# Optimization experiments

Measured on AMD Instinct MI355X. Metric: run time of the kernel, lower is better.

Reference implementation:

```python
import jax, jax.numpy as jnp
import numpy as np

N, D, H = 3072, 1152, 16
HD = D // H  # 72


def setup_inputs() -> dict:
    key = jax.random.key(0)
    ks = jax.random.split(key, 12)
    w = lambda k, shp: jax.random.normal(k, shp, dtype=jnp.float32) * 0.02
    return {
        "hidden_states": jax.random.normal(ks[0], (N, D), dtype=jnp.float32),
        "rotary_pos_emb": jax.random.normal(ks[1], (N, HD // 2), dtype=jnp.float32),
        "cu_seqlens": jnp.arange(5, dtype=jnp.int32) * (N // 4),
        "wq": w(ks[2], (D, D)), "bq": jnp.zeros((D,), jnp.float32),
        "wk": w(ks[3], (D, D)), "bk": jnp.zeros((D,), jnp.float32),
        "wv": w(ks[4], (D, D)), "bv": jnp.zeros((D,), jnp.float32),
        "wo": w(ks[5], (D, D)), "bo": jnp.zeros((D,), jnp.float32),
    }


def _rotate_half(x):
    x1, x2 = jnp.split(x, 2, axis=-1)
    return jnp.concatenate((-x2, x1), axis=-1)


def _apply_rope(t, freqs):
    # t: [N, H, HD], freqs: [N, HD//2]
    cos = jnp.concatenate([jnp.cos(freqs), jnp.cos(freqs)], axis=-1)[:, None, :]  # [N,1,HD]
    sin = jnp.concatenate([jnp.sin(freqs), jnp.sin(freqs)], axis=-1)[:, None, :]
    return (t.astype(jnp.float32) * cos + _rotate_half(t.astype(jnp.float32)) * sin).astype(t.dtype)


def reference(hidden_states, rotary_pos_emb, cu_seqlens, wq, bq, wk, bk, wv, bv, wo, bo):
    n = hidden_states.shape[0]
    q = (hidden_states @ wq.T + bq).reshape(n, H, HD)
    k = (hidden_states @ wk.T + bk).reshape(n, H, HD)
    v = (hidden_states @ wv.T + bv).reshape(n, H, HD)
    q = _apply_rope(q, rotary_pos_emb)
    k = _apply_rope(k, rotary_pos_emb)
    # block-diagonal mask: same segment id (from cu_seqlens) -> attend
    seg = jnp.searchsorted(cu_seqlens, jnp.arange(n), side="right")
    same = seg[:, None] == seg[None, :]  # [N, N]
    neg = jnp.finfo(q.dtype).min
    scores = jnp.einsum("qhd,khd->hqk", q, k) / jnp.sqrt(jnp.float32(HD)).astype(q.dtype)
    scores = scores + jnp.where(same, jnp.zeros((), q.dtype), neg)[None, :, :]
    attn = jax.nn.softmax(scores.astype(jnp.float32), axis=-1).astype(q.dtype)
    out = jnp.einsum("hqk,khd->qhd", attn, v).reshape(n, D)
    return out @ wo.T + bo
```

## Files before the change

kernel.cpp:

```cpp
#include <hip/hip_runtime.h>
#include <hip/hip_bf16.h>


typedef __attribute__((ext_vector_type(8))) __bf16 bf16x8;
typedef __attribute__((ext_vector_type(4))) float f32x4;
typedef __attribute__((ext_vector_type(8))) unsigned short u16x8;
typedef __attribute__((ext_vector_type(4))) unsigned short u16x4;

#define N_TOK 3072
#define DMODEL 1152
#define NH 16
#define HDIM 72
#define SEGLEN 768

__device__ __forceinline__ unsigned short bf16rn(float f) {
  union { float f; unsigned int u; } v; v.f = f;
  return (unsigned short)((v.u + 0x7fffu + ((v.u >> 16) & 1u)) >> 16);
}
__device__ __forceinline__ float bf2f(unsigned short u) {
  union { unsigned int i; float f; } v; v.i = ((unsigned int)u) << 16;
  return v.f;
}

#define GLOAD16(gsrc, ldst)                                                  \
  __builtin_amdgcn_global_load_lds(                                         \
      (const __attribute__((address_space(1))) unsigned int*)(gsrc),        \
      (__attribute__((address_space(3))) unsigned int*)(ldst), 16, 0, 0)

template <int N> __device__ __forceinline__ void waitcnt_vm() {
  if constexpr (N == 0) asm volatile("s_waitcnt vmcnt(0)" ::: "memory");
  else if constexpr (N == 2) asm volatile("s_waitcnt vmcnt(2)" ::: "memory");
  else if constexpr (N == 3) asm volatile("s_waitcnt vmcnt(3)" ::: "memory");
  else if constexpr (N == 4) asm volatile("s_waitcnt vmcnt(4)" ::: "memory");
}

__global__ __launch_bounds__(256) void prep_kernel(
    const float* __restrict__ hs,
    const float* __restrict__ wq, const float* __restrict__ wk,
    const float* __restrict__ wv, const float* __restrict__ wo,
    const float* __restrict__ bq, const float* __restrict__ bk,
    const float* __restrict__ bv,
    unsigned short* __restrict__ Xbf, unsigned short* __restrict__ Wqkv,
    unsigned short* __restrict__ Wo, float* __restrict__ biasqkv) {
  const int idx = blockIdx.x * 256 + threadIdx.x;
  const int stride = gridDim.x * 256;
  const int NX4 = (N_TOK * DMODEL) / 4;
  const int NW4 = (DMODEL * DMODEL) / 4;
  for (int i = idx; i < NX4; i += stride) {
    f32x4 v = ((const f32x4*)hs)[i];
    u16x4 o;
    for (int j = 0; j < 4; ++j) o[j] = bf16rn(v[j]);
    ((u16x4*)Xbf)[i] = o;
  }
  for (int i = idx; i < NW4; i += stride) {
    f32x4 a = ((const f32x4*)wq)[i];
    f32x4 b = ((const f32x4*)wk)[i];
    f32x4 c = ((const f32x4*)wv)[i];
    f32x4 d = ((const f32x4*)wo)[i];
    u16x4 oa, ob, oc, od;
    for (int j = 0; j < 4; ++j) {
      oa[j] = bf16rn(a[j]); ob[j] = bf16rn(b[j]);
      oc[j] = bf16rn(c[j]); od[j] = bf16rn(d[j]);
    }
    ((u16x4*)Wqkv)[i] = oa;
    ((u16x4*)(Wqkv + DMODEL * DMODEL))[i] = ob;
    ((u16x4*)(Wqkv + 2 * DMODEL * DMODEL))[i] = oc;
    ((u16x4*)Wo)[i] = od;
  }
  for (int i = idx; i < DMODEL; i += stride) {
    biasqkv[i] = bq[i];
    biasqkv[DMODEL + i] = bk[i];
    biasqkv[2 * DMODEL + i] = bv[i];
  }
}

template <int BM, int BN, int FM, int FN, bool OBF>
__global__ __launch_bounds__(256) void gemm_lds_kernel(
    const unsigned short* __restrict__ A, const unsigned short* __restrict__ B,
    const float* __restrict__ bias, void* __restrict__ Cout,
    int Nout, int K, int nbx) {
  __shared__ unsigned short As[3][BM * 32];
  __shared__ unsigned short Bs[3][BN * 32];
  const int t = threadIdx.x;
  const int lane = t & 63, wave = t >> 6;
  const int wr = wave >> 1, wc = wave & 1;
  const int g = lane >> 4, li = lane & 15;
  constexpr int LPS = BM / 64 + BN / 64;

  const int per = gridDim.x >> 3;
  const int gb = (blockIdx.x & 7) * per + (blockIdx.x >> 3);
  const int by = gb / nbx, bx = gb - by * nbx;
  const int bm = by * BM, bn = bx * BN;

  constexpr int LA = BM / 64;
  constexpr int LB = BN / 64;

  auto stage = [&](int buf, int kt) {
#pragma unroll
    for (int i = 0; i < LA; ++i) {
      const int s = i * 256 + t;
      const int row = s >> 2, cs = s & 3;
      const int gg = cs ^ ((row >> 1) & 3);
      GLOAD16(A + (long)(bm + row) * K + kt + gg * 8,
              &As[buf][(i * 256 + (t & ~63)) * 8]);
    }
#pragma unroll
    for (int i = 0; i < LB; ++i) {
      const int s = i * 256 + t;
      const int row = s >> 2, cs = s & 3;
      const int gg = cs ^ ((row >> 1) & 3);
      GLOAD16(B + (long)(bn + row) * K + kt + gg * 8,
              &Bs[buf][(i * 256 + (t & ~63)) * 8]);
    }
  };

  f32x4 acc[FM][FN];
#pragma unroll
  for (int i = 0; i < FM; ++i)
#pragma unroll
    for (int j = 0; j < FN; ++j) acc[i][j] = (f32x4)0.f;

  stage(0, 0);
  stage(1, 32);
  int cur = 0;
  const int nk = K / 32;
  for (int kt = 0; kt < nk; ++kt) {
    if (kt < nk - 1) waitcnt_vm<LPS>();
    else waitcnt_vm<0>();
    __builtin_amdgcn_s_barrier();
    if (kt + 2 < nk) {
      int nb = cur + 2; if (nb >= 3) nb -= 3;
      stage(nb, (kt + 2) * 32);
    }
    bf16x8 af[FM], bf[FN];
#pragma unroll
    for (int i = 0; i < FM; ++i) {
      const int r = wr * (BM / 2) + i * 16 + li;
      af[i] = *(const bf16x8*)&As[cur][r * 32 + ((g ^ ((r >> 1) & 3)) * 8)];
    }
#pragma unroll
    for (int j = 0; j < FN; ++j) {
      const int r = wc * (BN / 2) + j * 16 + li;
      bf[j] = *(const bf16x8*)&Bs[cur][r * 32 + ((g ^ ((r >> 1) & 3)) * 8)];
    }
    __builtin_amdgcn_s_setprio(1);
#pragma unroll
    for (int i = 0; i < FM; ++i)
#pragma unroll
      for (int j = 0; j < FN; ++j)
        acc[i][j] = __builtin_amdgcn_mfma_f32_16x16x32_bf16(af[i], bf[j],
                                                            acc[i][j], 0, 0, 0);
    __builtin_amdgcn_s_setprio(0);
    cur = (cur == 2) ? 0 : cur + 1;
  }

#pragma unroll
  for (int i = 0; i < FM; ++i) {
    const int row = bm + wr * (BM / 2) + i * 16 + g * 4;
#pragma unroll
    for (int j = 0; j < FN; ++j) {
      const int col = bn + wc * (BN / 2) + j * 16 + li;
      const float bb = bias[col];
#pragma unroll
      for (int r = 0; r < 4; ++r) {
        const float v = acc[i][j][r] + bb;
        if constexpr (OBF)
          ((unsigned short*)Cout)[(long)(row + r) * Nout + col] = bf16rn(v);
        else
          ((float*)Cout)[(long)(row + r) * Nout + col] = v;
      }
    }
  }
}

__global__ __launch_bounds__(256) void rope_pack_kernel(
    const unsigned short* __restrict__ qkv, const float* __restrict__ rope,
    unsigned short* __restrict__ Qp, unsigned short* __restrict__ Kp,
    unsigned short* __restrict__ Vt) {
  const int nb = blockIdx.x;
  const int h = blockIdx.y;
  const int n0 = nb * 64;
  const int t = threadIdx.x;
  const float qscale = 0.17002501f;
  __shared__ float cs[64][36], sn[64][36];
  __shared__ float vtile[72][65];

  for (int i = t; i < 64 * 36; i += 256) {
    const int n = i / 36, d = i % 36;
    const float f = rope[(long)(n0 + n) * 36 + d];
    cs[n][d] = __cosf(f);
    sn[n][d] = __sinf(f);
  }
  __syncthreads();

  for (int i = t; i < 64 * 9; i += 256) {
    const int n = i / 9, dq = (i % 9) * 4;
    const long base = (long)(n0 + n) * 3456 + h * HDIM;
    u16x4 q1 = *(const u16x4*)&qkv[base + dq];
    u16x4 q2 = *(const u16x4*)&qkv[base + dq + 36];
    u16x4 k1 = *(const u16x4*)&qkv[base + DMODEL + dq];
    u16x4 k2 = *(const u16x4*)&qkv[base + DMODEL + dq + 36];
    u16x4 oq1, oq2, ok1, ok2;
#pragma unroll
    for (int e = 0; e < 4; ++e) {
      const float c = cs[n][dq + e], s = sn[n][dq + e];
      float f1 = bf2f(q1[e]), f2 = bf2f(q2[e]);
      oq1[e] = bf16rn((f1 * c - f2 * s) * qscale);
      oq2[e] = bf16rn((f2 * c + f1 * s) * qscale);
      f1 = bf2f(k1[e]); f2 = bf2f(k2[e]);
      ok1[e] = bf16rn(f1 * c - f2 * s);
      ok2[e] = bf16rn(f2 * c + f1 * s);
    }
    const long ob = ((long)h * N_TOK + n0 + n) * 96;
    *(u16x4*)&Qp[ob + dq] = oq1;
    *(u16x4*)&Qp[ob + dq + 36] = oq2;
    *(u16x4*)&Kp[ob + dq] = ok1;
    *(u16x4*)&Kp[ob + dq + 36] = ok2;
  }
  for (int i = t; i < 64 * 6; i += 256) {
    const int n = i / 6, dp = HDIM + (i % 6) * 4;
    const long ob = ((long)h * N_TOK + n0 + n) * 96;
    *(u16x4*)&Qp[ob + dp] = (u16x4)0;
    *(u16x4*)&Kp[ob + dp] = (u16x4)0;
  }
  for (int i = t; i < 64 * 9; i += 256) {
    const int n = i / 9, dq = (i % 9) * 8;
    u16x8 v = *(const u16x8*)&qkv[(long)(n0 + n) * 3456 + 2 * DMODEL + h * HDIM + dq];
#pragma unroll
    for (int e = 0; e < 8; ++e) vtile[dq + e][n] = bf2f(v[e]);
  }
  __syncthreads();
  for (int i = t; i < 80 * 8; i += 256) {
    const int d = i / 8, nq = (i % 8) * 8;
    u16x8 o;
#pragma unroll
    for (int e = 0; e < 8; ++e)
      o[e] = (d < HDIM) ? bf16rn(vtile[d][nq + e])
                        : (d == HDIM ? (unsigned short)0x3F80
                                     : (unsigned short)0);
    *(u16x8*)&Vt[((long)h * 80 + d) * N_TOK + n0 + nq] = o;
  }
}

__global__ __launch_bounds__(256) void attn_kernel(
    const unsigned short* __restrict__ Qp, const unsigned short* __restrict__ Kp,
    const unsigned short* __restrict__ Vt, unsigned short* __restrict__ AO) {
  const int b = blockIdx.x;
  const int hs = b & 63, qt = b >> 6;
  const int h = hs >> 2, seg = hs & 3;
  const int t = threadIdx.x;
  const int lane = t & 63, w = t >> 6;
  const int g = lane >> 4, li = lane & 15;

  __shared__ unsigned short Ks[2][32 * 96];
  __shared__ unsigned short Vs[2][80 * 32];
  __shared__ unsigned short Ps[4][16][48];

  const int q0 = seg * SEGLEN + qt * 64;
  const unsigned short* kbase = Kp + ((long)h * N_TOK + seg * SEGLEN) * 96;
  const unsigned short* vbase = Vt + (long)h * 80 * N_TOK + seg * SEGLEN;

  auto stageK = [&](int buf, int koff) {
    {
      const int row = t / 12, c = t - row * 12;
      const int gg = c ^ ((row >> 1) & 3);
      GLOAD16(kbase + (long)(koff + row) * 96 + gg * 8,
              &Ks[buf][(t & ~63) * 8]);
    }
    if (t < 128) {
      const int s = 256 + t;
      const int row = s / 12, c = s - row * 12;
      const int gg = c ^ ((row >> 1) & 3);
      GLOAD16(kbase + (long)(koff + row) * 96 + gg * 8,
              &Ks[buf][(256 + (t & ~63)) * 8]);
    }
  };
  auto stageV = [&](int buf, int koff) {
    {
      const int row = t >> 2, ch = t & 3;
      const int gg = ch ^ ((row >> 1) & 3);
      GLOAD16(vbase + (long)row * N_TOK + koff + gg * 8,
              &Vs[buf][(t & ~63) * 8]);
    }
    if (t < 64) {
      const int s = 256 + t;
      const int row = s >> 2, ch = s & 3;
      const int gg = ch ^ ((row >> 1) & 3);
      GLOAD16(vbase + (long)row * N_TOK + koff + gg * 8,
              &Vs[buf][(256 + (t & ~63)) * 8]);
    }
  };

  bf16x8 aq[3];
  {
    const unsigned short* qsrc = Qp + ((long)h * N_TOK + q0 + w * 16 + li) * 96;
#pragma unroll
    for (int c = 0; c < 3; ++c)
      aq[c] = *(const bf16x8*)(qsrc + c * 32 + g * 8);
  }

  f32x4 accO[5];
#pragma unroll
  for (int j = 0; j < 5; ++j) accO[j] = (f32x4)0.f;

  stageK(0, 0);
  stageV(0, 0);
  int cur = 0;
  for (int kv = 0; kv < 24; ++kv) {
    __syncthreads();
    if (kv + 1 < 24) {
      stageK(cur ^ 1, (kv + 1) * 32);
      stageV(cur ^ 1, (kv + 1) * 32);
    }

    f32x4 sc[2];
#pragma unroll
    for (int f = 0; f < 2; ++f) sc[f] = (f32x4)0.f;
    __builtin_amdgcn_s_setprio(1);
#pragma unroll
    for (int c = 0; c < 3; ++c)
#pragma unroll
      for (int f = 0; f < 2; ++f) {
        const int kr = f * 16 + li;
        bf16x8 bk = *(const bf16x8*)
            &Ks[cur][kr * 96 + (((c * 4 + g) ^ ((kr >> 1) & 3)) * 8)];
        sc[f] = __builtin_amdgcn_mfma_f32_16x16x32_bf16(bk, aq[c], sc[f], 0, 0, 0);
      }
    __builtin_amdgcn_s_setprio(0);

#pragma unroll
    for (int f = 0; f < 2; ++f) {
      u16x4 pk;
#pragma unroll
      for (int r = 0; r < 4; ++r) pk[r] = bf16rn(exp2f(sc[f][r]));
      *(u16x4*)&Ps[w][li][f * 16 + g * 4] = pk;
    }

    {
      bf16x8 ap = *(const bf16x8*)&Ps[w][li][g * 8];
      __builtin_amdgcn_s_setprio(1);
#pragma unroll
      for (int j = 0; j < 5; ++j) {
        const int vr = j * 16 + li;
        bf16x8 bv = *(const bf16x8*)
            &Vs[cur][vr * 32 + ((g ^ ((vr >> 1) & 3)) * 8)];
        accO[j] = __builtin_amdgcn_mfma_f32_16x16x32_bf16(ap, bv, accO[j], 0, 0, 0);
      }
      __builtin_amdgcn_s_setprio(0);
    }
    cur ^= 1;
  }

  float rinv[4];
#pragma unroll
  for (int r = 0; r < 4; ++r)
    rinv[r] = 1.f / __shfl(accO[4][r], (lane & 48) + 8);

  const int hb = h * HDIM;
#pragma unroll
  for (int j = 0; j < 5; ++j) {
    const int d = j * 16 + li;
    if (d < HDIM) {
#pragma unroll
      for (int r = 0; r < 4; ++r) {
        const int n = q0 + w * 16 + g * 4 + r;
        AO[(long)n * DMODEL + hb + d] = bf16rn(accO[j][r] * rinv[r]);
      }
    }
  }
}

extern "C" void kernel_launch(void* const* d_in, const int* in_sizes, int n_in,
                              void* d_out, int out_size, void* d_ws,
                              size_t ws_size, hipStream_t stream) {
  const float* hs = (const float*)d_in[0];
  const float* rope = (const float*)d_in[1];
  const float* wq = (const float*)d_in[3];
  const float* bq = (const float*)d_in[4];
  const float* wk = (const float*)d_in[5];
  const float* bk = (const float*)d_in[6];
  const float* wv = (const float*)d_in[7];
  const float* bv = (const float*)d_in[8];
  const float* wo = (const float*)d_in[9];
  const float* bo = (const float*)d_in[10];
  float* out = (float*)d_out;
  char* ws = (char*)d_ws;

  unsigned short* Xbf = (unsigned short*)(ws + 0);
  unsigned short* Wqkv = (unsigned short*)(ws + 7077888);
  unsigned short* Wo = (unsigned short*)(ws + 15040512);
  float* biasqkv = (float*)(ws + 17694720);
  unsigned short* qkvb = (unsigned short*)(ws + 17708544);
  unsigned short* Qp = (unsigned short*)(ws + 38942208);
  unsigned short* Kp = (unsigned short*)(ws + 48379392);
  unsigned short* Vt = (unsigned short*)(ws + 57816576);
  unsigned short* AO = (unsigned short*)(ws + 65680896);

  prep_kernel<<<dim3(1024), dim3(256), 0, stream>>>(
      hs, wq, wk, wv, wo, bq, bk, bv, Xbf, Wqkv, Wo, biasqkv);
  gemm_lds_kernel<128, 128, 4, 4, true><<<dim3(648), dim3(256), 0, stream>>>(
      Xbf, Wqkv, biasqkv, qkvb, 3 * DMODEL, DMODEL, 27);
  rope_pack_kernel<<<dim3(48, 16), dim3(256), 0, stream>>>(
      qkvb, rope, Qp, Kp, Vt);
  attn_kernel<<<dim3(768), dim3(256), 0, stream>>>(Qp, Kp, Vt, AO);
  gemm_lds_kernel<64, 128, 2, 4, false><<<dim3(432), dim3(256), 0, stream>>>(
      AO, Wo, bo, out, DMODEL, DMODEL, 9);
}
```

Baseline: 110.3 us.

## Add dedicated 256x128 QKV GEMM kernel with interleaved prefetch and XCD remap

Replaces the generic 128x128 QKV projection GEMM with a specialized 512-thread kernel that uses 256x128 tiles, K-step 64, and double-buffered LDS with XOR swizzle. Global-to-LDS prefetches for the next tile are interleaved between MFMA groups, and s_setprio raises priority around the MFMA bursts. Blocks are remapped per XCD so that each chiplet works on neighbouring tiles. The aim is higher arithmetic intensity and fewer blocks (324 instead of 648), in exchange for more LDS per block and lower occupancy.

```diff
diff --git a/kernel.cpp b/kernel.cpp
--- a/kernel.cpp
+++ b/kernel.cpp
@@ -29,6 +29,7 @@
 
 template <int N> __device__ __forceinline__ void waitcnt_vm() {
   if constexpr (N == 0) asm volatile("s_waitcnt vmcnt(0)" ::: "memory");
+  else if constexpr (N == 1) asm volatile("s_waitcnt vmcnt(1)" ::: "memory");
   else if constexpr (N == 2) asm volatile("s_waitcnt vmcnt(2)" ::: "memory");
   else if constexpr (N == 3) asm volatile("s_waitcnt vmcnt(3)" ::: "memory");
   else if constexpr (N == 4) asm volatile("s_waitcnt vmcnt(4)" ::: "memory");
@@ -74,6 +75,137 @@
   }
 }
 
+__global__ __launch_bounds__(512) void gemm_qkv_kernel(
+    const unsigned short* __restrict__ A, const unsigned short* __restrict__ B,
+    const float* __restrict__ bias, unsigned short* __restrict__ C) {
+  constexpr int K = DMODEL;
+  constexpr int NOUT = 3 * DMODEL;
+  __shared__ unsigned short As[2][256 * 64];
+  __shared__ unsigned short Bs[2][128 * 64];
+  const int t = threadIdx.x;
+  const int lane = t & 63, w = t >> 6;
+  const int wr = w >> 1, wc = w & 1;
+  const int g = lane >> 4, li = lane & 15;
+
+  const int orig = blockIdx.x;
+  const int xcd = orig & 7, pos = orig >> 3;
+  const int gb = (xcd < 4 ? xcd * 41 : 164 + (xcd - 4) * 40) + pos;
+  const int by = gb % 12, bx = gb / 12;
+  const int bm = by * 256, bn = bx * 128;
+
+  auto stageA = [&](int buf, int ko, int q) {
+    const int s = q * 512 + t;
+    const int row = s >> 3, ch = s & 7;
+    GLOAD16(A + (long)(bm + row) * K + ko + ((ch ^ (row & 7)) * 8),
+            &As[buf][(q * 512 + (t & ~63)) * 8]);
+  };
+  auto stageB = [&](int buf, int ko, int hf) {
+    const int s = hf * 512 + t;
+    const int row = s >> 3, ch = s & 7;
+    GLOAD16(B + (long)(bn + row) * K + ko + ((ch ^ (row & 7)) * 8),
+            &Bs[buf][(hf * 512 + (t & ~63)) * 8]);
+  };
+  auto rdA = [&](int buf, int i, int ks) -> bf16x8 {
+    const int r = wr * 64 + i * 16 + li;
+    return *(const bf16x8*)&As[buf][r * 64 + ((((ks << 2) + g) ^ (r & 7)) * 8)];
+  };
+  auto rdB = [&](int buf, int j, int ks) -> bf16x8 {
+    const int r = wc * 64 + j * 16 + li;
+    return *(const bf16x8*)&Bs[buf][r * 64 + ((((ks << 2) + g) ^ (r & 7)) * 8)];
+  };
+
+  f32x4 acc[4][4];
+#pragma unroll
+  for (int i = 0; i < 4; ++i)
+#pragma unroll
+    for (int j = 0; j < 4; ++j) acc[i][j] = (f32x4)0.f;
+
+  stageA(0, 0, 0); stageA(0, 0, 1); stageA(0, 0, 2); stageA(0, 0, 3);
+  stageB(0, 0, 0); stageB(0, 0, 1);
+
+  for (int kt = 0; kt < 18; ++kt) {
+    const int buf = kt & 1;
+    const bool pf = kt < 17;
+    const int ko = (kt + 1) * 64;
+    if (pf) {
+      stageA(buf ^ 1, ko, 0);
+      stageA(buf ^ 1, ko, 1);
+      waitcnt_vm<2>();
+    } else {
+      waitcnt_vm<0>();
+    }
+    __builtin_amdgcn_s_barrier();
+
+    bf16x8 b0, b1, b2, b3, a0, a1;
+    b0 = rdB(buf, 0, 0); b1 = rdB(buf, 1, 0);
+    b2 = rdB(buf, 2, 0); b3 = rdB(buf, 3, 0);
+    a0 = rdA(buf, 0, 0); a1 = rdA(buf, 1, 0);
+    if (pf) stageA(buf ^ 1, ko, 2);
+    __builtin_amdgcn_s_setprio(1);
+    acc[0][0] = __builtin_amdgcn_mfma_f32_16x16x32_bf16(a0, b0, acc[0][0], 0, 0, 0);
+    acc[0][1] = __builtin_amdgcn_mfma_f32_16x16x32_bf16(a0, b1, acc[0][1], 0, 0, 0);
+    acc[0][2] = __builtin_amdgcn_mfma_f32_16x16x32_bf16(a0, b2, acc[0][2], 0, 0, 0);
+    acc[0][3] = __builtin_amdgcn_mfma_f32_16x16x32_bf16(a0, b3, acc[0][3], 0, 0, 0);
+    acc[1][0] = __builtin_amdgcn_mfma_f32_16x16x32_bf16(a1, b0, acc[1][0], 0, 0, 0);
+    acc[1][1] = __builtin_amdgcn_mfma_f32_16x16x32_bf16(a1, b1, acc[1][1], 0, 0, 0);
+    acc[1][2] = __builtin_amdgcn_mfma_f32_16x16x32_bf16(a1, b2, acc[1][2], 0, 0, 0);
+    acc[1][3] = __builtin_amdgcn_mfma_f32_16x16x32_bf16(a1, b3, acc[1][3], 0, 0, 0);
+    __builtin_amdgcn_s_setprio(0);
+    a0 = rdA(buf, 2, 0); a1 = rdA(buf, 3, 0);
+    if (pf) stageA(buf ^ 1, ko, 3);
+    __builtin_amdgcn_s_setprio(1);
+    acc[2][0] = __builtin_amdgcn_mfma_f32_16x16x32_bf16(a0, b0, acc[2][0], 0, 0, 0);
+    acc[2][1] = __builtin_amdgcn_mfma_f32_16x16x32_bf16(a0, b1, acc[2][1], 0, 0, 0);
+    acc[2][2] = __builtin_amdgcn_mfma_f32_16x16x32_bf16(a0, b2, acc[2][2], 0, 0, 0);
+    acc[2][3] = __builtin_amdgcn_mfma_f32_16x16x32_bf16(a0, b3, acc[2][3], 0, 0, 0);
+    acc[3][0] = __builtin_amdgcn_mfma_f32_16x16x32_bf16(a1, b0, acc[3][0], 0, 0, 0);
+    acc[3][1] = __builtin_amdgcn_mfma_f32_16x16x32_bf16(a1, b1, acc[3][1], 0, 0, 0);
+    acc[3][2] = __builtin_amdgcn_mfma_f32_16x16x32_bf16(a1, b2, acc[3][2], 0, 0, 0);
+    acc[3][3] = __builtin_amdgcn_mfma_f32_16x16x32_bf16(a1, b3, acc[3][3], 0, 0, 0);
+    __builtin_amdgcn_s_setprio(0);
+    b0 = rdB(buf, 0, 1); b1 = rdB(buf, 1, 1);
+    b2 = rdB(buf, 2, 1); b3 = rdB(buf, 3, 1);
+    a0 = rdA(buf, 0, 1); a1 = rdA(buf, 1, 1);
+    if (pf) stageB(buf ^ 1, ko, 0);
+    __builtin_amdgcn_s_setprio(1);
+    acc[0][0] = __builtin_amdgcn_mfma_f32_16x16x32_bf16(a0, b0, acc[0][0], 0, 0, 0);
+    acc[0][1] = __builtin_amdgcn_mfma_f32_16x16x32_bf16(a0, b1, acc[0][1], 0, 0, 0);
+    acc[0][2] = __builtin_amdgcn_mfma_f32_16x16x32_bf16(a0, b2, acc[0][2], 0, 0, 0);
+    acc[0][3] = __builtin_amdgcn_mfma_f32_16x16x32_bf16(a0, b3, acc[0][3], 0, 0, 0);
+    acc[1][0] = __builtin_amdgcn_mfma_f32_16x16x32_bf16(a1, b0, acc[1][0], 0, 0, 0);
+    acc[1][1] = __builtin_amdgcn_mfma_f32_16x16x32_bf16(a1, b1, acc[1][1], 0, 0, 0);
+    acc[1][2] = __builtin_amdgcn_mfma_f32_16x16x32_bf16(a1, b2, acc[1][2], 0, 0, 0);
+    acc[1][3] = __builtin_amdgcn_mfma_f32_16x16x32_bf16(a1, b3, acc[1][3], 0, 0, 0);
+    __builtin_amdgcn_s_setprio(0);
+    a0 = rdA(buf, 2, 1); a1 = rdA(buf, 3, 1);
+    if (pf) stageB(buf ^ 1, ko, 1);
+    __builtin_amdgcn_s_setprio(1);
+    acc[2][0] = __builtin_amdgcn_mfma_f32_16x16x32_bf16(a0, b0, acc[2][0], 0, 0, 0);
+    acc[2][1] = __builtin_amdgcn_mfma_f32_16x16x32_bf16(a0, b1, acc[2][1], 0, 0, 0);
+    acc[2][2] = __builtin_amdgcn_mfma_f32_16x16x32_bf16(a0, b2, acc[2][2], 0, 0, 0);
+    acc[2][3] = __builtin_amdgcn_mfma_f32_16x16x32_bf16(a0, b3, acc[2][3], 0, 0, 0);
+    acc[3][0] = __builtin_amdgcn_mfma_f32_16x16x32_bf16(a1, b0, acc[3][0], 0, 0, 0);
+    acc[3][1] = __builtin_amdgcn_mfma_f32_16x16x32_bf16(a1, b1, acc[3][1], 0, 0, 0);
+    acc[3][2] = __builtin_amdgcn_mfma_f32_16x16x32_bf16(a1, b2, acc[3][2], 0, 0, 0);
+    acc[3][3] = __builtin_amdgcn_mfma_f32_16x16x32_bf16(a1, b3, acc[3][3], 0, 0, 0);
+    __builtin_amdgcn_s_setprio(0);
+    __builtin_amdgcn_s_barrier();
+  }
+
+#pragma unroll
+  for (int i = 0; i < 4; ++i) {
+    const int row = bm + wr * 64 + i * 16 + g * 4;
+#pragma unroll
+    for (int j = 0; j < 4; ++j) {
+      const int col = bn + wc * 64 + j * 16 + li;
+      const float bb = bias[col];
+#pragma unroll
+      for (int r = 0; r < 4; ++r)
+        C[(long)(row + r) * NOUT + col] = bf16rn(acc[i][j][r] + bb);
+    }
+  }
+}
+
 template <int BM, int BN, int FM, int FN, bool OBF>
 __global__ __launch_bounds__(256) void gemm_lds_kernel(
     const unsigned short* __restrict__ A, const unsigned short* __restrict__ B,
@@ -398,8 +530,8 @@
 
   prep_kernel<<<dim3(1024), dim3(256), 0, stream>>>(
       hs, wq, wk, wv, wo, bq, bk, bv, Xbf, Wqkv, Wo, biasqkv);
-  gemm_lds_kernel<128, 128, 4, 4, true><<<dim3(648), dim3(256), 0, stream>>>(
-      Xbf, Wqkv, biasqkv, qkvb, 3 * DMODEL, DMODEL, 27);
+  gemm_qkv_kernel<<<dim3(324), dim3(512), 0, stream>>>(
+      Xbf, Wqkv, biasqkv, qkvb);
   rope_pack_kernel<<<dim3(48, 16), dim3(256), 0, stream>>>(
       qkvb, rope, Qp, Kp, Vt);
   attn_kernel<<<dim3(768), dim3(256), 0, stream>>>(Qp, Kp, Vt, AO);
```

Result: slower. 133.5 us (+21.0%).

## Double KV tile to 64 and pass P via ds_bpermute instead of LDS

Applied to the files above, without the earlier changes.

The attention kernel now processes 64 keys per iteration instead of 32, halving the loop trip count and the number of barriers. The V tile uses a wider row with an 8-way XOR swizzle. The softmax probabilities are packed with v_cvt_pk_bf16_f32 and moved into MFMA A-operand layout with ds_bpermute, replacing the LDS round-trip through a P buffer. In exchange it uses more LDS for the K/V double buffers and issues more cross-lane permute instructions per tile.

```diff
diff --git a/kernel.cpp b/kernel.cpp
--- a/kernel.cpp
+++ b/kernel.cpp
@@ -6,6 +6,7 @@
 typedef __attribute__((ext_vector_type(4))) float f32x4;
 typedef __attribute__((ext_vector_type(8))) unsigned short u16x8;
 typedef __attribute__((ext_vector_type(4))) unsigned short u16x4;
+typedef __attribute__((ext_vector_type(4))) unsigned int u32x4;
 
 #define N_TOK 3072
 #define DMODEL 1152
@@ -252,42 +253,38 @@
   const int lane = t & 63, w = t >> 6;
   const int g = lane >> 4, li = lane & 15;
 
-  __shared__ unsigned short Ks[2][32 * 96];
-  __shared__ unsigned short Vs[2][80 * 32];
-  __shared__ unsigned short Ps[4][16][48];
+  __shared__ unsigned short Ks[2][64 * 96];
+  __shared__ unsigned short Vs[2][80 * 64];
 
   const int q0 = seg * SEGLEN + qt * 64;
   const unsigned short* kbase = Kp + ((long)h * N_TOK + seg * SEGLEN) * 96;
   const unsigned short* vbase = Vt + (long)h * 80 * N_TOK + seg * SEGLEN;
 
   auto stageK = [&](int buf, int koff) {
-    {
-      const int row = t / 12, c = t - row * 12;
-      const int gg = c ^ ((row >> 1) & 3);
-      GLOAD16(kbase + (long)(koff + row) * 96 + gg * 8,
-              &Ks[buf][(t & ~63) * 8]);
-    }
-    if (t < 128) {
-      const int s = 256 + t;
+#pragma unroll
+    for (int i = 0; i < 3; ++i) {
+      const int s = i * 256 + t;
       const int row = s / 12, c = s - row * 12;
       const int gg = c ^ ((row >> 1) & 3);
       GLOAD16(kbase + (long)(koff + row) * 96 + gg * 8,
-              &Ks[buf][(256 + (t & ~63)) * 8]);
+              &Ks[buf][(i * 256 + (t & ~63)) * 8]);
     }
   };
   auto stageV = [&](int buf, int koff) {
-    {
-      const int row = t >> 2, ch = t & 3;
-      const int gg = ch ^ ((row >> 1) & 3);
+#pragma unroll
+    for (int i = 0; i < 2; ++i) {
+      const int s = i * 256 + t;
+      const int row = s >> 3, ch = s & 7;
+      const int gg = ch ^ (row & 7);
       GLOAD16(vbase + (long)row * N_TOK + koff + gg * 8,
-              &Vs[buf][(t & ~63) * 8]);
-    }
-    if (t < 64) {
-      const int s = 256 + t;
-      const int row = s >> 2, ch = s & 3;
-      const int gg = ch ^ ((row >> 1) & 3);
+              &Vs[buf][(i * 256 + (t & ~63)) * 8]);
+    }
+    if (t < 128) {
+      const int s = 512 + t;
+      const int row = s >> 3, ch = s & 7;
+      const int gg = ch ^ (row & 7);
       GLOAD16(vbase + (long)row * N_TOK + koff + gg * 8,
-              &Vs[buf][(256 + (t & ~63)) * 8]);
+              &Vs[buf][(512 + (t & ~63)) * 8]);
     }
   };
 
@@ -299,6 +296,10 @@
       aq[c] = *(const bf16x8*)(qsrc + c * 32 + g * 8);
   }
 
+  const int a0 = (li + 32 * (g & 1)) << 2;
+  const int a1 = a0 + 64;
+  const bool glow = (g < 2);
+
   f32x4 accO[5];
 #pragma unroll
   for (int j = 0; j < 5; ++j) accO[j] = (f32x4)0.f;
@@ -306,21 +307,21 @@
   stageK(0, 0);
   stageV(0, 0);
   int cur = 0;
-  for (int kv = 0; kv < 24; ++kv) {
+  for (int kv = 0; kv < 12; ++kv) {
     __syncthreads();
-    if (kv + 1 < 24) {
-      stageK(cur ^ 1, (kv + 1) * 32);
-      stageV(cur ^ 1, (kv + 1) * 32);
-    }
-
-    f32x4 sc[2];
-#pragma unroll
-    for (int f = 0; f < 2; ++f) sc[f] = (f32x4)0.f;
+    if (kv + 1 < 12) {
+      stageK(cur ^ 1, (kv + 1) * 64);
+      stageV(cur ^ 1, (kv + 1) * 64);
+    }
+
+    f32x4 sc[4];
+#pragma unroll
+    for (int f = 0; f < 4; ++f) sc[f] = (f32x4)0.f;
     __builtin_amdgcn_s_setprio(1);
 #pragma unroll
     for (int c = 0; c < 3; ++c)
 #pragma unroll
-      for (int f = 0; f < 2; ++f) {
+      for (int f = 0; f < 4; ++f) {
         const int kr = f * 16 + li;
         bf16x8 bk = *(const bf16x8*)
             &Ks[cur][kr * 96 + (((c * 4 + g) ^ ((kr >> 1) & 3)) * 8)];
@@ -328,26 +329,43 @@
       }
     __builtin_amdgcn_s_setprio(0);
 
-#pragma unroll
-    for (int f = 0; f < 2; ++f) {
-      u16x4 pk;
-#pragma unroll
-      for (int r = 0; r < 4; ++r) pk[r] = bf16rn(exp2f(sc[f][r]));
-      *(u16x4*)&Ps[w][li][f * 16 + g * 4] = pk;
-    }
-
-    {
-      bf16x8 ap = *(const bf16x8*)&Ps[w][li][g * 8];
-      __builtin_amdgcn_s_setprio(1);
+    unsigned int pk[4][2];
+#pragma unroll
+    for (int f = 0; f < 4; ++f) {
+      float e0 = exp2f(sc[f][0]), e1 = exp2f(sc[f][1]);
+      float e2 = exp2f(sc[f][2]), e3 = exp2f(sc[f][3]);
+      asm("v_cvt_pk_bf16_f32 %0, %1, %2" : "=v"(pk[f][0]) : "v"(e0), "v"(e1));
+      asm("v_cvt_pk_bf16_f32 %0, %1, %2" : "=v"(pk[f][1]) : "v"(e2), "v"(e3));
+    }
+
+    __builtin_amdgcn_s_setprio(1);
+#pragma unroll
+    for (int c = 0; c < 2; ++c) {
+      u32x4 apv;
+      {
+        int t0 = __builtin_amdgcn_ds_bpermute(a0, (int)pk[2 * c][0]);
+        int t1 = __builtin_amdgcn_ds_bpermute(a0, (int)pk[2 * c + 1][0]);
+        apv[0] = (unsigned int)(glow ? t0 : t1);
+        t0 = __builtin_amdgcn_ds_bpermute(a0, (int)pk[2 * c][1]);
+        t1 = __builtin_amdgcn_ds_bpermute(a0, (int)pk[2 * c + 1][1]);
+        apv[1] = (unsigned int)(glow ? t0 : t1);
+        t0 = __builtin_amdgcn_ds_bpermute(a1, (int)pk[2 * c][0]);
+        t1 = __builtin_amdgcn_ds_bpermute(a1, (int)pk[2 * c + 1][0]);
+        apv[2] = (unsigned int)(glow ? t0 : t1);
+        t0 = __builtin_amdgcn_ds_bpermute(a1, (int)pk[2 * c][1]);
+        t1 = __builtin_amdgcn_ds_bpermute(a1, (int)pk[2 * c + 1][1]);
+        apv[3] = (unsigned int)(glow ? t0 : t1);
+      }
+      bf16x8 ap = *(bf16x8*)&apv;
 #pragma unroll
       for (int j = 0; j < 5; ++j) {
         const int vr = j * 16 + li;
         bf16x8 bv = *(const bf16x8*)
-            &Vs[cur][vr * 32 + ((g ^ ((vr >> 1) & 3)) * 8)];
+            &Vs[cur][vr * 64 + ((((c * 4 + g) ^ (vr & 7))) * 8)];
         accO[j] = __builtin_amdgcn_mfma_f32_16x16x32_bf16(ap, bv, accO[j], 0, 0, 0);
       }
-      __builtin_amdgcn_s_setprio(0);
-    }
+    }
+    __builtin_amdgcn_s_setprio(0);
     cur ^= 1;
   }
 
```

After: 109.1 us. No clear change (-1.1%).
